# Kernel optimization log

Measured on AMD Instinct MI355X. Metric: run time of the kernel, lower is better.

Reference implementation:

```python
import jax, jax.numpy as jnp
import numpy as np

N_NODES = 100000
N_EDGES = 1600000
IN_DIM = 256
OUT_DIM = 64


def setup_inputs() -> dict:
    key = jax.random.key(0)
    k1, k2, k3, k4, k5 = jax.random.split(key, 5)
    x = jax.random.normal(k1, (N_NODES, IN_DIM), dtype=jnp.float32)
    # Glorot-normal-like kernel
    kernel = jax.random.normal(k2, (IN_DIM, OUT_DIM), dtype=jnp.float32) * jnp.sqrt(2.0 / (IN_DIM + OUT_DIM))
    adj_vals = jax.random.uniform(k3, (N_EDGES,), dtype=jnp.float32)
    adj_rows = jnp.sort(jax.random.randint(k4, (N_EDGES,), 0, N_NODES, dtype=jnp.int32))
    adj_cols = jax.random.randint(k5, (N_EDGES,), 0, N_NODES, dtype=jnp.int32)
    return {"x": x, "kernel": kernel, "adj_vals": adj_vals,
            "adj_rows": adj_rows, "adj_cols": adj_cols}


def reference(x, kernel, adj_vals, adj_rows, adj_cols):
    # Dropout is identity at inference (training=False / rate=0.0).
    h = x @ kernel                                  # [N, OUT_DIM] dense GEMM
    # SpMM: out[r] = sum_{e: rows[e]==r} vals[e] * h[cols[e]]
    msgs = adj_vals[:, None] * h[adj_cols]          # [E, OUT_DIM] gather + scale
    agg = jax.ops.segment_sum(msgs, adj_rows, num_segments=x.shape[0])
    return jax.nn.relu(agg)
```

## Files before the change

kernel.cpp:

```cpp
#include <hip/hip_runtime.h>

#define N_NODES 100000
#define N_EDGES 1600000
#define IN_DIM  256
#define OUT_DIM 64

typedef __attribute__((ext_vector_type(8))) short bf16x8;
typedef __attribute__((ext_vector_type(4))) float f32x4;

__device__ __forceinline__ short f2bf(float f) {
    union { float f; unsigned u; } v; v.f = f;
    unsigned r = v.u + 0x7fffu + ((v.u >> 16) & 1u);
    return (short)(r >> 16);
}
__device__ __forceinline__ float bf2f(unsigned short us) {
    union { unsigned u; float f; } v; v.u = ((unsigned)us) << 16;
    return v.f;
}

#define WB_STRIDE 264

__global__ __launch_bounds__(256)
void gcn_gemm_mfma(const float* __restrict__ x,
                   const float* __restrict__ w,
                   unsigned short* __restrict__ hb)
{
    __shared__ short wb[OUT_DIM * WB_STRIDE];

    for (int idx = threadIdx.x; idx < IN_DIM * OUT_DIM; idx += 256) {
        int k = idx >> 6;
        int n = idx & 63;
        wb[n * WB_STRIDE + k] = f2bf(w[idx]);
    }
    __syncthreads();

    const int lane = threadIdx.x & 63;
    const int wv   = threadIdx.x >> 6;
    const int r0   = blockIdx.x * 64 + wv * 16;

    const int arow   = r0 + (lane & 15);
    const int arow_c = arow < N_NODES ? arow : N_NODES - 1;
    const int kbase  = (lane >> 4) << 3;
    const float* xr  = x + (size_t)arow_c * IN_DIM + kbase;

    const int nlo = lane & 15;
    const short* wb0 = &wb[(0  + nlo) * WB_STRIDE + kbase];
    const short* wb1 = &wb[(16 + nlo) * WB_STRIDE + kbase];
    const short* wb2 = &wb[(32 + nlo) * WB_STRIDE + kbase];
    const short* wb3 = &wb[(48 + nlo) * WB_STRIDE + kbase];

    f32x4 acc0 = {0.f, 0.f, 0.f, 0.f};
    f32x4 acc1 = {0.f, 0.f, 0.f, 0.f};
    f32x4 acc2 = {0.f, 0.f, 0.f, 0.f};
    f32x4 acc3 = {0.f, 0.f, 0.f, 0.f};

#pragma unroll
    for (int k0 = 0; k0 < IN_DIM; k0 += 32) {
        float4 f0 = *(const float4*)(xr + k0);
        float4 f1 = *(const float4*)(xr + k0 + 4);
        bf16x8 a;
        a[0] = f2bf(f0.x); a[1] = f2bf(f0.y); a[2] = f2bf(f0.z); a[3] = f2bf(f0.w);
        a[4] = f2bf(f1.x); a[5] = f2bf(f1.y); a[6] = f2bf(f1.z); a[7] = f2bf(f1.w);

        bf16x8 b0 = *(const bf16x8*)(wb0 + k0);
        bf16x8 b1 = *(const bf16x8*)(wb1 + k0);
        bf16x8 b2 = *(const bf16x8*)(wb2 + k0);
        bf16x8 b3 = *(const bf16x8*)(wb3 + k0);

        acc0 = __builtin_amdgcn_mfma_f32_16x16x32_bf16(a, b0, acc0, 0, 0, 0);
        acc1 = __builtin_amdgcn_mfma_f32_16x16x32_bf16(a, b1, acc1, 0, 0, 0);
        acc2 = __builtin_amdgcn_mfma_f32_16x16x32_bf16(a, b2, acc2, 0, 0, 0);
        acc3 = __builtin_amdgcn_mfma_f32_16x16x32_bf16(a, b3, acc3, 0, 0, 0);
    }

    const int crow0 = r0 + ((lane >> 4) << 2);
#pragma unroll
    for (int rr = 0; rr < 4; ++rr) {
        int row = crow0 + rr;
        if (row < N_NODES) {
            unsigned short* hp = hb + (size_t)row * OUT_DIM + nlo;
            hp[0]  = (unsigned short)f2bf(acc0[rr]);
            hp[16] = (unsigned short)f2bf(acc1[rr]);
            hp[32] = (unsigned short)f2bf(acc2[rr]);
            hp[48] = (unsigned short)f2bf(acc3[rr]);
        }
    }
}

#define SPMM_ROWS_PER_BLOCK 64
#define SEG_CAP 2048

__device__ __forceinline__ int lower_bound_rows(const int* __restrict__ rows, int val)
{
    int lo = 0, hi = N_EDGES;
    while (lo < hi) {
        int mid = (lo + hi) >> 1;
        if (rows[mid] < val) lo = mid + 1; else hi = mid;
    }
    return lo;
}

__global__ __launch_bounds__(256)
void gcn_spmm_relu_kernel(const unsigned short* __restrict__ hb,
                          const float* __restrict__ vals,
                          const int* __restrict__ rows,
                          const int* __restrict__ cols,
                          float* __restrict__ out)
{
    __shared__ int   starts[SPMM_ROWS_PER_BLOCK + 1];
    __shared__ float s_vals[SEG_CAP];
    __shared__ int   s_cols[SEG_CAP];

    const int row0 = blockIdx.x * SPMM_ROWS_PER_BLOCK;
    const int t    = threadIdx.x;

    if (t <= SPMM_ROWS_PER_BLOCK) {
        int target = row0 + t;
        starts[t] = (target >= N_NODES) ? N_EDGES : lower_bound_rows(rows, target);
    }
    __syncthreads();

    const int seg0   = starts[0];
    const int segEnd = starts[SPMM_ROWS_PER_BLOCK];
    const int segLen = segEnd - seg0;
    const bool fits  = (segLen <= SEG_CAP);

    if (fits) {
        for (int i = t; i < segLen; i += 256) {
            s_vals[i] = vals[seg0 + i];
            s_cols[i] = cols[seg0 + i];
        }
    }
    __syncthreads();

    const int lane = t & 63;
    const int wv   = t >> 6;

    for (int rr = wv; rr < SPMM_ROWS_PER_BLOCK; rr += 4) {
        int r = row0 + rr;
        if (r >= N_NODES) break;
        int s = starts[rr]     - seg0;
        int e = starts[rr + 1] - seg0;
        float acc0 = 0.f, acc1 = 0.f, acc2 = 0.f, acc3 = 0.f;
        if (fits) {
            int ei = s;
            for (; ei + 3 < e; ei += 4) {
                float v0 = s_vals[ei];     int c0 = s_cols[ei];
                float v1 = s_vals[ei + 1]; int c1 = s_cols[ei + 1];
                float v2 = s_vals[ei + 2]; int c2 = s_cols[ei + 2];
                float v3 = s_vals[ei + 3]; int c3 = s_cols[ei + 3];
                float h0 = bf2f(hb[(size_t)c0 * OUT_DIM + lane]);
                float h1 = bf2f(hb[(size_t)c1 * OUT_DIM + lane]);
                float h2 = bf2f(hb[(size_t)c2 * OUT_DIM + lane]);
                float h3 = bf2f(hb[(size_t)c3 * OUT_DIM + lane]);
                acc0 = fmaf(v0, h0, acc0);
                acc1 = fmaf(v1, h1, acc1);
                acc2 = fmaf(v2, h2, acc2);
                acc3 = fmaf(v3, h3, acc3);
            }
            for (; ei < e; ++ei) {
                acc0 = fmaf(s_vals[ei], bf2f(hb[(size_t)s_cols[ei] * OUT_DIM + lane]), acc0);
            }
        } else {
            for (int ei = s; ei < e; ++ei) {
                float v = vals[seg0 + ei];
                int   c = cols[seg0 + ei];
                acc0 = fmaf(v, bf2f(hb[(size_t)c * OUT_DIM + lane]), acc0);
            }
        }
        out[(size_t)r * OUT_DIM + lane] = fmaxf((acc0 + acc1) + (acc2 + acc3), 0.f);
    }
}

extern "C" void kernel_launch(void* const* d_in, const int* in_sizes, int n_in,
                              void* d_out, int out_size, void* d_ws, size_t ws_size,
                              hipStream_t stream)
{
    const float* x    = (const float*)d_in[0];
    const float* w    = (const float*)d_in[1];
    const float* vals = (const float*)d_in[2];
    const int*   rows = (const int*)d_in[3];
    const int*   cols = (const int*)d_in[4];
    float*       out  = (float*)d_out;
    unsigned short* hb = (unsigned short*)d_ws;

    const int gemm_grid = (N_NODES + 63) / 64;
    gcn_gemm_mfma<<<gemm_grid, 256, 0, stream>>>(x, w, hb);

    const int spmm_grid = (N_NODES + SPMM_ROWS_PER_BLOCK - 1) / SPMM_ROWS_PER_BLOCK;
    gcn_spmm_relu_kernel<<<spmm_grid, 256, 0, stream>>>(hb, vals, rows, cols, out);
}
```

Baseline: 79.92 us.

## Split each SpMM row across half-waves processing two edges with packed bf16 loads

Each wavefront now handles two edges per step: each half-wave of 32 lanes loads a 32-bit pair of bf16 features for one edge, and the partial sums are combined with a cross-half shuffle before the ReLU and a float2 store. Edge values and columns are packed into a single uint2 shared array. Rows per block drop to 32, with a matching shared capacity, which increases the grid size. The aim is to halve the serial edge loop length per row and widen gather loads. The cost is an extra shuffle, idle lanes on odd edge counts, and more binary searches because there are more blocks.

```diff
diff --git a/kernel.cpp b/kernel.cpp
--- a/kernel.cpp
+++ b/kernel.cpp
@@ -12,10 +12,6 @@
     union { float f; unsigned u; } v; v.f = f;
     unsigned r = v.u + 0x7fffu + ((v.u >> 16) & 1u);
     return (short)(r >> 16);
-}
-__device__ __forceinline__ float bf2f(unsigned short us) {
-    union { unsigned u; float f; } v; v.u = ((unsigned)us) << 16;
-    return v.f;
 }
 
 #define WB_STRIDE 264
@@ -87,8 +83,8 @@
     }
 }
 
-#define SPMM_ROWS_PER_BLOCK 64
-#define SEG_CAP 2048
+#define SPMM_ROWS_PER_BLOCK 32
+#define SEG_CAP 1024
 
 __device__ __forceinline__ int lower_bound_rows(const int* __restrict__ rows, int val)
 {
@@ -108,8 +104,7 @@
                           float* __restrict__ out)
 {
     __shared__ int   starts[SPMM_ROWS_PER_BLOCK + 1];
-    __shared__ float s_vals[SEG_CAP];
-    __shared__ int   s_cols[SEG_CAP];
+    __shared__ uint2 s_ec[SEG_CAP];
 
     const int row0 = blockIdx.x * SPMM_ROWS_PER_BLOCK;
     const int t    = threadIdx.x;
@@ -121,54 +116,80 @@
     __syncthreads();
 
     const int seg0   = starts[0];
-    const int segEnd = starts[SPMM_ROWS_PER_BLOCK];
-    const int segLen = segEnd - seg0;
+    const int segLen = starts[SPMM_ROWS_PER_BLOCK] - seg0;
     const bool fits  = (segLen <= SEG_CAP);
 
     if (fits) {
         for (int i = t; i < segLen; i += 256) {
-            s_vals[i] = vals[seg0 + i];
-            s_cols[i] = cols[seg0 + i];
+            s_ec[i] = make_uint2(__float_as_uint(vals[seg0 + i]),
+                                 (unsigned)cols[seg0 + i]);
         }
     }
     __syncthreads();
 
     const int lane = t & 63;
     const int wv   = t >> 6;
+    const int half = lane >> 5;
+    const int sub  = lane & 31;
 
     for (int rr = wv; rr < SPMM_ROWS_PER_BLOCK; rr += 4) {
-        int r = row0 + rr;
-        if (r >= N_NODES) break;
-        int s = starts[rr]     - seg0;
-        int e = starts[rr + 1] - seg0;
-        float acc0 = 0.f, acc1 = 0.f, acc2 = 0.f, acc3 = 0.f;
+        const int r = row0 + rr;
+        const int s = starts[rr]     - seg0;
+        const int e = starts[rr + 1] - seg0;
+        const int n  = e - s;
+        const int tc = (n + 1) >> 1;
+
+        float aL0 = 0.f, aH0 = 0.f, aL1 = 0.f, aH1 = 0.f;
+        float aL2 = 0.f, aH2 = 0.f, aL3 = 0.f, aH3 = 0.f;
+
         if (fits) {
-            int ei = s;
-            for (; ei + 3 < e; ei += 4) {
-                float v0 = s_vals[ei];     int c0 = s_cols[ei];
-                float v1 = s_vals[ei + 1]; int c1 = s_cols[ei + 1];
-                float v2 = s_vals[ei + 2]; int c2 = s_cols[ei + 2];
-                float v3 = s_vals[ei + 3]; int c3 = s_cols[ei + 3];
-                float h0 = bf2f(hb[(size_t)c0 * OUT_DIM + lane]);
-                float h1 = bf2f(hb[(size_t)c1 * OUT_DIM + lane]);
-                float h2 = bf2f(hb[(size_t)c2 * OUT_DIM + lane]);
-                float h3 = bf2f(hb[(size_t)c3 * OUT_DIM + lane]);
-                acc0 = fmaf(v0, h0, acc0);
-                acc1 = fmaf(v1, h1, acc1);
-                acc2 = fmaf(v2, h2, acc2);
-                acc3 = fmaf(v3, h3, acc3);
-            }
-            for (; ei < e; ++ei) {
-                acc0 = fmaf(s_vals[ei], bf2f(hb[(size_t)s_cols[ei] * OUT_DIM + lane]), acc0);
-            }
+#define STEP_L(i_, aL_, aH_)                                                   \
+            {                                                                  \
+                int ei    = s + 2 * (i_) + half;                               \
+                bool ok   = ei < e;                                            \
+                int eidx  = ok ? ei : e - 1;                                   \
+                uint2 vc  = s_ec[eidx];                                        \
+                float v   = ok ? __uint_as_float(vc.x) : 0.f;                  \
+                unsigned hx = *(const unsigned*)(hb + (size_t)vc.y * OUT_DIM   \
+                                                 + 2u * sub);                  \
+                aL_ = fmaf(v, __uint_as_float(hx << 16), aL_);                 \
+                aH_ = fmaf(v, __uint_as_float(hx & 0xffff0000u), aH_);         \
+            }
+            int i = 0;
+            for (; i + 3 < tc; i += 4) {
+                STEP_L(i + 0, aL0, aH0)
+                STEP_L(i + 1, aL1, aH1)
+                STEP_L(i + 2, aL2, aH2)
+                STEP_L(i + 3, aL3, aH3)
+            }
+            for (; i < tc; ++i) {
+                STEP_L(i, aL0, aH0)
+            }
+#undef STEP_L
         } else {
-            for (int ei = s; ei < e; ++ei) {
-                float v = vals[seg0 + ei];
-                int   c = cols[seg0 + ei];
-                acc0 = fmaf(v, bf2f(hb[(size_t)c * OUT_DIM + lane]), acc0);
-            }
-        }
-        out[(size_t)r * OUT_DIM + lane] = fmaxf((acc0 + acc1) + (acc2 + acc3), 0.f);
+            for (int i = 0; i < tc; ++i) {
+                int ei   = s + 2 * i + half;
+                bool ok  = ei < e;
+                int eidx = (ok ? ei : e - 1) + seg0;
+                float v  = ok ? vals[eidx] : 0.f;
+                unsigned c = (unsigned)cols[eidx];
+                unsigned hx = *(const unsigned*)(hb + (size_t)c * OUT_DIM + 2u * sub);
+                aL0 = fmaf(v, __uint_as_float(hx << 16), aL0);
+                aH0 = fmaf(v, __uint_as_float(hx & 0xffff0000u), aH0);
+            }
+        }
+
+        float lo = (aL0 + aL1) + (aL2 + aL3);
+        float hi = (aH0 + aH1) + (aH2 + aH3);
+        lo += __shfl_xor(lo, 32);
+        hi += __shfl_xor(hi, 32);
+
+        if (half == 0) {
+            float2 o;
+            o.x = fmaxf(lo, 0.f);
+            o.y = fmaxf(hi, 0.f);
+            *(float2*)(out + (size_t)r * OUT_DIM + 2u * sub) = o;
+        }
     }
 }
 
```

Result: no change. 78.47 us (-1.8%).

## Reorder SpMM edges into column bands and process two edges per wave

Applied to the files above, without the earlier changes.

Inside each 64-row block, the SpMM kernel now counting-sorts edges by column band (col>>14) using shared-memory atomics. It then walks all rows band by band, so gathers from h stay within a limited address range at any one time, which should improve L2 locality. Each wave handles 16 rows with register accumulators. Each half-wave processes alternate edges and loads two bf16 values per lane, then combines the halves with a cross-lane shuffle. The cost is extra preprocessing passes, repeated binary searches, atomics and more register pressure.

```diff
diff --git a/kernel.cpp b/kernel.cpp
--- a/kernel.cpp
+++ b/kernel.cpp
@@ -12,10 +12,6 @@
     union { float f; unsigned u; } v; v.f = f;
     unsigned r = v.u + 0x7fffu + ((v.u >> 16) & 1u);
     return (short)(r >> 16);
-}
-__device__ __forceinline__ float bf2f(unsigned short us) {
-    union { unsigned u; float f; } v; v.u = ((unsigned)us) << 16;
-    return v.f;
 }
 
 #define WB_STRIDE 264
@@ -88,7 +84,9 @@
 }
 
 #define SPMM_ROWS_PER_BLOCK 64
-#define SEG_CAP 2048
+#define SEG_CAP 1536
+#define BAND_SHIFT 14
+#define NB 7
 
 __device__ __forceinline__ int lower_bound_rows(const int* __restrict__ rows, int val)
 {
@@ -100,75 +98,138 @@
     return lo;
 }
 
-__global__ __launch_bounds__(256)
-void gcn_spmm_relu_kernel(const unsigned short* __restrict__ hb,
-                          const float* __restrict__ vals,
-                          const int* __restrict__ rows,
-                          const int* __restrict__ cols,
-                          float* __restrict__ out)
-{
-    __shared__ int   starts[SPMM_ROWS_PER_BLOCK + 1];
-    __shared__ float s_vals[SEG_CAP];
-    __shared__ int   s_cols[SEG_CAP];
+__global__ __launch_bounds__(256, 2)
+void gcn_spmm_band(const unsigned short* __restrict__ hb,
+                   const float* __restrict__ vals,
+                   const int* __restrict__ rows,
+                   const int* __restrict__ cols,
+                   float* __restrict__ out)
+{
+    __shared__ int   s_starts[SPMM_ROWS_PER_BLOCK + 1];
+    __shared__ uint2 s_ec2[SEG_CAP];
+    __shared__ int   s_cnt [SPMM_ROWS_PER_BLOCK][8];
+    __shared__ int   s_bofs[SPMM_ROWS_PER_BLOCK][8];
+    __shared__ int   s_cur [SPMM_ROWS_PER_BLOCK][8];
 
     const int row0 = blockIdx.x * SPMM_ROWS_PER_BLOCK;
     const int t    = threadIdx.x;
 
     if (t <= SPMM_ROWS_PER_BLOCK) {
         int target = row0 + t;
-        starts[t] = (target >= N_NODES) ? N_EDGES : lower_bound_rows(rows, target);
-    }
+        s_starts[t] = (target >= N_NODES) ? N_EDGES : lower_bound_rows(rows, target);
+    }
+    for (int i = t; i < SPMM_ROWS_PER_BLOCK * 8; i += 256) ((int*)s_cnt)[i] = 0;
     __syncthreads();
 
-    const int seg0   = starts[0];
-    const int segEnd = starts[SPMM_ROWS_PER_BLOCK];
-    const int segLen = segEnd - seg0;
+    const int seg0   = s_starts[0];
+    const int segLen = s_starts[SPMM_ROWS_PER_BLOCK] - seg0;
     const bool fits  = (segLen <= SEG_CAP);
+
+    const int lane = t & 63;
+    const int wv   = t >> 6;
+    const int half = lane >> 5;
+    const int sub  = lane & 31;
 
     if (fits) {
         for (int i = t; i < segLen; i += 256) {
-            s_vals[i] = vals[seg0 + i];
-            s_cols[i] = cols[seg0 + i];
-        }
-    }
-    __syncthreads();
-
-    const int lane = t & 63;
-    const int wv   = t >> 6;
-
-    for (int rr = wv; rr < SPMM_ROWS_PER_BLOCK; rr += 4) {
-        int r = row0 + rr;
-        if (r >= N_NODES) break;
-        int s = starts[rr]     - seg0;
-        int e = starts[rr + 1] - seg0;
-        float acc0 = 0.f, acc1 = 0.f, acc2 = 0.f, acc3 = 0.f;
-        if (fits) {
-            int ei = s;
-            for (; ei + 3 < e; ei += 4) {
-                float v0 = s_vals[ei];     int c0 = s_cols[ei];
-                float v1 = s_vals[ei + 1]; int c1 = s_cols[ei + 1];
-                float v2 = s_vals[ei + 2]; int c2 = s_cols[ei + 2];
-                float v3 = s_vals[ei + 3]; int c3 = s_cols[ei + 3];
-                float h0 = bf2f(hb[(size_t)c0 * OUT_DIM + lane]);
-                float h1 = bf2f(hb[(size_t)c1 * OUT_DIM + lane]);
-                float h2 = bf2f(hb[(size_t)c2 * OUT_DIM + lane]);
-                float h3 = bf2f(hb[(size_t)c3 * OUT_DIM + lane]);
-                acc0 = fmaf(v0, h0, acc0);
-                acc1 = fmaf(v1, h1, acc1);
-                acc2 = fmaf(v2, h2, acc2);
-                acc3 = fmaf(v3, h3, acc3);
-            }
-            for (; ei < e; ++ei) {
-                acc0 = fmaf(s_vals[ei], bf2f(hb[(size_t)s_cols[ei] * OUT_DIM + lane]), acc0);
-            }
-        } else {
-            for (int ei = s; ei < e; ++ei) {
-                float v = vals[seg0 + ei];
-                int   c = cols[seg0 + ei];
-                acc0 = fmaf(v, bf2f(hb[(size_t)c * OUT_DIM + lane]), acc0);
-            }
-        }
-        out[(size_t)r * OUT_DIM + lane] = fmaxf((acc0 + acc1) + (acc2 + acc3), 0.f);
+            int gi = seg0 + i;
+            int b  = cols[gi] >> BAND_SHIFT;
+            int lo = 0, hi = SPMM_ROWS_PER_BLOCK - 1;
+            while (lo < hi) {
+                int mid = (lo + hi + 1) >> 1;
+                if (s_starts[mid] <= gi) lo = mid; else hi = mid - 1;
+            }
+            atomicAdd(&s_cnt[lo][b], 1);
+        }
+        __syncthreads();
+        if (t < SPMM_ROWS_PER_BLOCK) {
+            int acc = 0;
+#pragma unroll
+            for (int b = 0; b < 8; ++b) {
+                s_bofs[t][b] = acc;
+                s_cur [t][b] = acc;
+                acc += s_cnt[t][b];
+            }
+        }
+        __syncthreads();
+        for (int i = t; i < segLen; i += 256) {
+            int gi = seg0 + i;
+            int c  = cols[gi];
+            float v = vals[gi];
+            int b  = c >> BAND_SHIFT;
+            int lo = 0, hi = SPMM_ROWS_PER_BLOCK - 1;
+            while (lo < hi) {
+                int mid = (lo + hi + 1) >> 1;
+                if (s_starts[mid] <= gi) lo = mid; else hi = mid - 1;
+            }
+            int rbase = s_starts[lo] - seg0;
+            int pos   = rbase + atomicAdd(&s_cur[lo][b], 1);
+            s_ec2[pos] = make_uint2(__float_as_uint(v), (unsigned)c);
+        }
+        __syncthreads();
+
+        float accL[16], accH[16];
+#pragma unroll
+        for (int rr = 0; rr < 16; ++rr) { accL[rr] = 0.f; accH[rr] = 0.f; }
+
+        for (int b = 0; b < NB; ++b) {
+#pragma unroll
+            for (int rr = 0; rr < 16; ++rr) {
+                const int r     = wv * 16 + rr;
+                const int rbase = s_starts[r] - seg0;
+                const int bs    = rbase + s_bofs[r][b];
+                const int n     = s_cnt[r][b];
+                const int tc    = (n + 1) >> 1;
+                for (int i = 0; i < tc; ++i) {
+                    int  k  = 2 * i + half;
+                    bool ok = k < n;
+                    uint2 vc = s_ec2[ok ? (bs + k) : bs];
+                    float v  = ok ? __uint_as_float(vc.x) : 0.f;
+                    unsigned hx = *(const unsigned*)(hb + (size_t)vc.y * OUT_DIM + 2u * sub);
+                    accL[rr] = fmaf(v, __uint_as_float(hx << 16),         accL[rr]);
+                    accH[rr] = fmaf(v, __uint_as_float(hx & 0xffff0000u), accH[rr]);
+                }
+            }
+        }
+
+#pragma unroll
+        for (int rr = 0; rr < 16; ++rr) {
+            int r = row0 + wv * 16 + rr;
+            float lo = accL[rr] + __shfl_xor(accL[rr], 32);
+            float hi = accH[rr] + __shfl_xor(accH[rr], 32);
+            if (half == 0 && r < N_NODES) {
+                float2 o;
+                o.x = fmaxf(lo, 0.f);
+                o.y = fmaxf(hi, 0.f);
+                *(float2*)(out + (size_t)r * OUT_DIM + 2u * sub) = o;
+            }
+        }
+    } else {
+        for (int rr = wv; rr < SPMM_ROWS_PER_BLOCK; rr += 4) {
+            int r = row0 + rr;
+            if (r >= N_NODES) break;
+            int s = s_starts[rr], e = s_starts[rr + 1];
+            int n = e - s, tc = (n + 1) >> 1;
+            float aL = 0.f, aH = 0.f;
+            for (int i = 0; i < tc; ++i) {
+                int ei  = s + 2 * i + half;
+                bool ok = ei < e;
+                int idx = ok ? ei : s;
+                float v = ok ? vals[idx] : 0.f;
+                unsigned c  = (unsigned)cols[idx];
+                unsigned hx = *(const unsigned*)(hb + (size_t)c * OUT_DIM + 2u * sub);
+                aL = fmaf(v, __uint_as_float(hx << 16),         aL);
+                aH = fmaf(v, __uint_as_float(hx & 0xffff0000u), aH);
+            }
+            aL += __shfl_xor(aL, 32);
+            aH += __shfl_xor(aH, 32);
+            if (half == 0) {
+                float2 o;
+                o.x = fmaxf(aL, 0.f);
+                o.y = fmaxf(aH, 0.f);
+                *(float2*)(out + (size_t)r * OUT_DIM + 2u * sub) = o;
+            }
+        }
     }
 }
 
@@ -188,5 +249,5 @@
     gcn_gemm_mfma<<<gemm_grid, 256, 0, stream>>>(x, w, hb);
 
     const int spmm_grid = (N_NODES + SPMM_ROWS_PER_BLOCK - 1) / SPMM_ROWS_PER_BLOCK;
-    gcn_spmm_relu_kernel<<<spmm_grid, 256, 0, stream>>>(hb, vals, rows, cols, out);
-}
+    gcn_spmm_band<<<spmm_grid, 256, 0, stream>>>(hb, vals, rows, cols, out);
+}
```

After: 115.9 us. 1.45x slower.

## Precompute row starts and gather 16-byte rows per lane group in SpMM

Applied to the files above, without the earlier changes.

Moves the per-row binary search into a separate build_row_starts kernel that writes row offsets to workspace. The SpMM is restructured so each 8-lane group fetches a full 128-byte bf16 row of h with 16-byte loads, 8 edges at a time, and the partial sums are reduced with xor shuffles. Edge values and columns are packed into one shared uint2 array, and the tile shrinks to 32 rows per block. The aim is fewer, wider gather transactions and less redundant search work, at the cost of an extra launch and shuffle reductions.

```diff
diff --git a/kernel.cpp b/kernel.cpp
--- a/kernel.cpp
+++ b/kernel.cpp
@@ -7,15 +7,12 @@
 
 typedef __attribute__((ext_vector_type(8))) short bf16x8;
 typedef __attribute__((ext_vector_type(4))) float f32x4;
+typedef __attribute__((ext_vector_type(4))) unsigned u32x4;
 
 __device__ __forceinline__ short f2bf(float f) {
     union { float f; unsigned u; } v; v.f = f;
     unsigned r = v.u + 0x7fffu + ((v.u >> 16) & 1u);
     return (short)(r >> 16);
-}
-__device__ __forceinline__ float bf2f(unsigned short us) {
-    union { unsigned u; float f; } v; v.u = ((unsigned)us) << 16;
-    return v.f;
 }
 
 #define WB_STRIDE 264
@@ -56,8 +53,8 @@
 
 #pragma unroll
     for (int k0 = 0; k0 < IN_DIM; k0 += 32) {
-        float4 f0 = *(const float4*)(xr + k0);
-        float4 f1 = *(const float4*)(xr + k0 + 4);
+        f32x4 f0 = *(const f32x4*)(xr + k0);
+        f32x4 f1 = *(const f32x4*)(xr + k0 + 4);
         bf16x8 a;
         a[0] = f2bf(f0.x); a[1] = f2bf(f0.y); a[2] = f2bf(f0.z); a[3] = f2bf(f0.w);
         a[4] = f2bf(f1.x); a[5] = f2bf(f1.y); a[6] = f2bf(f1.z); a[7] = f2bf(f1.w);
@@ -87,89 +84,141 @@
     }
 }
 
-#define SPMM_ROWS_PER_BLOCK 64
-#define SEG_CAP 2048
-
-__device__ __forceinline__ int lower_bound_rows(const int* __restrict__ rows, int val)
-{
+__global__ __launch_bounds__(256)
+void build_row_starts(const int* __restrict__ rows, int* __restrict__ starts)
+{
+    int r = blockIdx.x * 256 + threadIdx.x;
+    if (r > N_NODES) return;
     int lo = 0, hi = N_EDGES;
     while (lo < hi) {
         int mid = (lo + hi) >> 1;
-        if (rows[mid] < val) lo = mid + 1; else hi = mid;
-    }
-    return lo;
-}
-
-__global__ __launch_bounds__(256)
-void gcn_spmm_relu_kernel(const unsigned short* __restrict__ hb,
-                          const float* __restrict__ vals,
-                          const int* __restrict__ rows,
-                          const int* __restrict__ cols,
-                          float* __restrict__ out)
+        if (rows[mid] < r) lo = mid + 1; else hi = mid;
+    }
+    starts[r] = lo;
+}
+
+#define SPMM_ROWS_PER_BLOCK 32
+#define SEG_CAP 1024
+
+__global__ __launch_bounds__(256, 2)
+void gcn_spmm_wide(const unsigned short* __restrict__ hb,
+                   const float* __restrict__ vals,
+                   const int* __restrict__ row_starts,
+                   const int* __restrict__ cols,
+                   float* __restrict__ out)
 {
     __shared__ int   starts[SPMM_ROWS_PER_BLOCK + 1];
-    __shared__ float s_vals[SEG_CAP];
-    __shared__ int   s_cols[SEG_CAP];
+    __shared__ uint2 s_ec[SEG_CAP];
 
     const int row0 = blockIdx.x * SPMM_ROWS_PER_BLOCK;
     const int t    = threadIdx.x;
 
     if (t <= SPMM_ROWS_PER_BLOCK) {
-        int target = row0 + t;
-        starts[t] = (target >= N_NODES) ? N_EDGES : lower_bound_rows(rows, target);
+        starts[t] = row_starts[row0 + t];
     }
     __syncthreads();
 
     const int seg0   = starts[0];
-    const int segEnd = starts[SPMM_ROWS_PER_BLOCK];
-    const int segLen = segEnd - seg0;
+    const int segLen = starts[SPMM_ROWS_PER_BLOCK] - seg0;
     const bool fits  = (segLen <= SEG_CAP);
 
     if (fits) {
         for (int i = t; i < segLen; i += 256) {
-            s_vals[i] = vals[seg0 + i];
-            s_cols[i] = cols[seg0 + i];
+            s_ec[i] = make_uint2(__float_as_uint(vals[seg0 + i]),
+                                 (unsigned)cols[seg0 + i]);
         }
     }
     __syncthreads();
 
     const int lane = t & 63;
     const int wv   = t >> 6;
+    const int grp  = lane >> 3;
+    const int sl   = lane & 7;
+    const unsigned off16 = (unsigned)(sl << 4);
+    const char* hbase = (const char*)hb;
+
+#define FMA8(v_, h_)                                                        \
+    {                                                                       \
+        a0 = fmaf(v_, __uint_as_float((h_).x << 16),         a0);           \
+        a1 = fmaf(v_, __uint_as_float((h_).x & 0xffff0000u), a1);           \
+        a2 = fmaf(v_, __uint_as_float((h_).y << 16),         a2);           \
+        a3 = fmaf(v_, __uint_as_float((h_).y & 0xffff0000u), a3);           \
+        a4 = fmaf(v_, __uint_as_float((h_).z << 16),         a4);           \
+        a5 = fmaf(v_, __uint_as_float((h_).z & 0xffff0000u), a5);           \
+        a6 = fmaf(v_, __uint_as_float((h_).w << 16),         a6);           \
+        a7 = fmaf(v_, __uint_as_float((h_).w & 0xffff0000u), a7);           \
+    }
 
     for (int rr = wv; rr < SPMM_ROWS_PER_BLOCK; rr += 4) {
-        int r = row0 + rr;
-        if (r >= N_NODES) break;
-        int s = starts[rr]     - seg0;
-        int e = starts[rr + 1] - seg0;
-        float acc0 = 0.f, acc1 = 0.f, acc2 = 0.f, acc3 = 0.f;
+        const int r    = row0 + rr;
+        const int s    = starts[rr]     - seg0;
+        const int n    = starts[rr + 1] - seg0 - s;
+        const int tc8  = n >> 3;
+        const int tail = n & 7;
+
+        float a0 = 0.f, a1 = 0.f, a2 = 0.f, a3 = 0.f;
+        float a4 = 0.f, a5 = 0.f, a6 = 0.f, a7 = 0.f;
+
         if (fits) {
-            int ei = s;
-            for (; ei + 3 < e; ei += 4) {
-                float v0 = s_vals[ei];     int c0 = s_cols[ei];
-                float v1 = s_vals[ei + 1]; int c1 = s_cols[ei + 1];
-                float v2 = s_vals[ei + 2]; int c2 = s_cols[ei + 2];
-                float v3 = s_vals[ei + 3]; int c3 = s_cols[ei + 3];
-                float h0 = bf2f(hb[(size_t)c0 * OUT_DIM + lane]);
-                float h1 = bf2f(hb[(size_t)c1 * OUT_DIM + lane]);
-                float h2 = bf2f(hb[(size_t)c2 * OUT_DIM + lane]);
-                float h3 = bf2f(hb[(size_t)c3 * OUT_DIM + lane]);
-                acc0 = fmaf(v0, h0, acc0);
-                acc1 = fmaf(v1, h1, acc1);
-                acc2 = fmaf(v2, h2, acc2);
-                acc3 = fmaf(v3, h3, acc3);
-            }
-            for (; ei < e; ++ei) {
-                acc0 = fmaf(s_vals[ei], bf2f(hb[(size_t)s_cols[ei] * OUT_DIM + lane]), acc0);
+            int i = 0;
+            for (; i + 2 <= tc8; i += 2) {
+                uint2 vcA = s_ec[s + (i + 0) * 8 + grp];
+                uint2 vcB = s_ec[s + (i + 1) * 8 + grp];
+                u32x4 hA = *(const u32x4*)(hbase + ((vcA.y << 7) + off16));
+                u32x4 hB = *(const u32x4*)(hbase + ((vcB.y << 7) + off16));
+                float vA = __uint_as_float(vcA.x);
+                float vB = __uint_as_float(vcB.x);
+                FMA8(vA, hA)
+                FMA8(vB, hB)
+            }
+            if (i < tc8) {
+                uint2 vc = s_ec[s + i * 8 + grp];
+                u32x4 h  = *(const u32x4*)(hbase + ((vc.y << 7) + off16));
+                float v  = __uint_as_float(vc.x);
+                FMA8(v, h)
+            }
+            if (tail) {
+                bool ok  = grp < tail;
+                int eidx = s + tc8 * 8 + (ok ? grp : 0);
+                uint2 vc = s_ec[eidx];
+                float v  = ok ? __uint_as_float(vc.x) : 0.f;
+                u32x4 h  = *(const u32x4*)(hbase + ((vc.y << 7) + off16));
+                FMA8(v, h)
             }
         } else {
-            for (int ei = s; ei < e; ++ei) {
-                float v = vals[seg0 + ei];
-                int   c = cols[seg0 + ei];
-                acc0 = fmaf(v, bf2f(hb[(size_t)c * OUT_DIM + lane]), acc0);
-            }
-        }
-        out[(size_t)r * OUT_DIM + lane] = fmaxf((acc0 + acc1) + (acc2 + acc3), 0.f);
-    }
+            for (int i = 0; i < tc8 + (tail ? 1 : 0); ++i) {
+                int base = s + i * 8;
+                int lim  = (i < tc8) ? 8 : tail;
+                bool ok  = grp < lim;
+                int gi   = seg0 + base + (ok ? grp : 0);
+                float v  = ok ? vals[gi] : 0.f;
+                unsigned c = (unsigned)cols[gi];
+                u32x4 h  = *(const u32x4*)(hbase + ((c << 7) + off16));
+                FMA8(v, h)
+            }
+        }
+
+        a0 += __shfl_xor(a0, 8);  a0 += __shfl_xor(a0, 16);  a0 += __shfl_xor(a0, 32);
+        a1 += __shfl_xor(a1, 8);  a1 += __shfl_xor(a1, 16);  a1 += __shfl_xor(a1, 32);
+        a2 += __shfl_xor(a2, 8);  a2 += __shfl_xor(a2, 16);  a2 += __shfl_xor(a2, 32);
+        a3 += __shfl_xor(a3, 8);  a3 += __shfl_xor(a3, 16);  a3 += __shfl_xor(a3, 32);
+        a4 += __shfl_xor(a4, 8);  a4 += __shfl_xor(a4, 16);  a4 += __shfl_xor(a4, 32);
+        a5 += __shfl_xor(a5, 8);  a5 += __shfl_xor(a5, 16);  a5 += __shfl_xor(a5, 32);
+        a6 += __shfl_xor(a6, 8);  a6 += __shfl_xor(a6, 16);  a6 += __shfl_xor(a6, 32);
+        a7 += __shfl_xor(a7, 8);  a7 += __shfl_xor(a7, 16);  a7 += __shfl_xor(a7, 32);
+
+        if (grp == 0) {
+            f32x4 o0, o1;
+            o0.x = fmaxf(a0, 0.f); o0.y = fmaxf(a1, 0.f);
+            o0.z = fmaxf(a2, 0.f); o0.w = fmaxf(a3, 0.f);
+            o1.x = fmaxf(a4, 0.f); o1.y = fmaxf(a5, 0.f);
+            o1.z = fmaxf(a6, 0.f); o1.w = fmaxf(a7, 0.f);
+            float* op = out + (size_t)r * OUT_DIM + (sl << 3);
+            *(f32x4*)(op)     = o0;
+            *(f32x4*)(op + 4) = o1;
+        }
+    }
+#undef FMA8
 }
 
 extern "C" void kernel_launch(void* const* d_in, const int* in_sizes, int n_in,
@@ -182,11 +231,15 @@
     const int*   rows = (const int*)d_in[3];
     const int*   cols = (const int*)d_in[4];
     float*       out  = (float*)d_out;
+
     unsigned short* hb = (unsigned short*)d_ws;
+    int* row_starts = (int*)((char*)d_ws + (size_t)N_NODES * OUT_DIM * sizeof(unsigned short));
+
+    build_row_starts<<<(N_NODES + 1 + 255) / 256, 256, 0, stream>>>(rows, row_starts);
 
     const int gemm_grid = (N_NODES + 63) / 64;
     gcn_gemm_mfma<<<gemm_grid, 256, 0, stream>>>(x, w, hb);
 
     const int spmm_grid = (N_NODES + SPMM_ROWS_PER_BLOCK - 1) / SPMM_ROWS_PER_BLOCK;
-    gcn_spmm_relu_kernel<<<spmm_grid, 256, 0, stream>>>(hb, vals, rows, cols, out);
-}
+    gcn_spmm_wide<<<spmm_grid, 256, 0, stream>>>(hb, vals, row_starts, cols, out);
+}
```

Result: faster. 75.05 us (-6.1%).
